# Optimization experiments

Measured on AMD Instinct MI355X. Metric: run time of the kernel, lower is better.

## Reference

```python
import jax, jax.numpy as jnp
import numpy as np

D = 1024
H = 16
FFN = 4096
B = 4
S = 1024
EPS = 1e-12
NEG = -1e9


def _layernorm(x, gamma, beta):
    mean = x.mean(-1, keepdims=True)
    var = ((x - mean) ** 2).mean(-1, keepdims=True)  # biased var, matches unbiased=False
    return gamma * (x - mean) * jax.lax.rsqrt(var + EPS) + beta


def setup_inputs() -> dict:
    key = jax.random.key(0)
    ks = jax.random.split(key, 16)
    s_in = 1.0 / np.sqrt(D)
    s_ff = 1.0 / np.sqrt(FFN)
    return {
        "x": jax.random.normal(ks[0], (B, S, D), dtype=jnp.float32),
        "mask": jax.random.randint(ks[1], (B, H, S), 0, 2) > 0,  # bernoulli(0.5) key mask
        "Wqkv": jax.random.uniform(ks[2], (3 * D, D), minval=-s_in, maxval=s_in),
        "bqkv": jax.random.uniform(ks[3], (3 * D,), minval=-s_in, maxval=s_in),
        "Wo": jax.random.uniform(ks[4], (D, D), minval=-s_in, maxval=s_in),
        "bo": jax.random.uniform(ks[5], (D,), minval=-s_in, maxval=s_in),
        "W1": jax.random.uniform(ks[6], (FFN, D), minval=-s_in, maxval=s_in),
        "b1": jax.random.uniform(ks[7], (FFN,), minval=-s_in, maxval=s_in),
        "W2": jax.random.uniform(ks[8], (D, FFN), minval=-s_ff, maxval=s_ff),
        "b2": jax.random.uniform(ks[9], (D,), minval=-s_ff, maxval=s_ff),
        "g1": jnp.ones((D,), jnp.float32),
        "be1": jnp.zeros((D,), jnp.float32),
        "g2": jnp.ones((D,), jnp.float32),
        "be2": jnp.zeros((D,), jnp.float32),
    }


def reference(x, mask, Wqkv, bqkv, Wo, bo, W1, b1, W2, b2, g1, be1, g2, be2):
    b, s, _ = x.shape
    hd = D // H
    scale = hd ** -0.5

    # --- ProbSparseSelfAttention (dropout in eval mode) ---
    qkv = x @ Wqkv.T + bqkv                                   # [b, s, 3D]
    q, k, v = jnp.split(qkv, 3, axis=-1)
    q = q.reshape(b, s, H, hd).transpose(0, 2, 1, 3)          # [b, h, s, d]
    k = k.reshape(b, s, H, hd).transpose(0, 2, 1, 3)
    v = v.reshape(b, s, H, hd).transpose(0, 2, 1, 3)
    scores = jnp.einsum('bhid,bhjd->bhij', q * scale, k)      # [b, h, s, s]
    scores = jnp.where(mask[:, :, None, :], scores, NEG)      # mask keys (broadcast over i)
    attn = jax.nn.softmax(scores, axis=-1)
    ctx = jnp.einsum('bhij,bhjd->bhid', attn, v)
    ctx = ctx.transpose(0, 2, 1, 3).reshape(b, s, D)
    attn_out = ctx @ Wo.T + bo

    # residual + LayerNorm 1
    h = _layernorm(attn_out + x, g1, be1)

    # --- FFN ---
    ff = jax.nn.relu(h @ W1.T + b1) @ W2.T + b2

    # residual + LayerNorm 2
    return _layernorm(ff + h, g2, be2)
```

## Files before the change

### kernel.cpp

```cpp
#include <hip/hip_runtime.h>

#define DDIM 1024
#define FFN_DIM 4096
#define SS 1024
#define MTOK 4096

typedef __bf16 bf16x8 __attribute__((ext_vector_type(8)));
typedef float f32x4 __attribute__((ext_vector_type(4)));
typedef unsigned short ushort4v __attribute__((ext_vector_type(4)));
typedef unsigned short ushort8v __attribute__((ext_vector_type(8)));

__device__ __forceinline__ unsigned short f2bf(float f) {
    union { float f; unsigned u; } x;
    x.f = f;
    unsigned r = x.u + 0x7FFFu + ((x.u >> 16) & 1u);
    return (unsigned short)(r >> 16);
}
__device__ __forceinline__ float bf2f(unsigned short u) {
    union { unsigned u; float f; } x;
    x.u = (unsigned)u << 16;
    return x.f;
}

__device__ __forceinline__ int swz(int off) {
    return off ^ ((((off >> 7) & 7) ^ ((off >> 10) & 1)) << 4);
}

__device__ __forceinline__ void gload_lds16(const void* g, void* l) {
    __builtin_amdgcn_global_load_lds(
        (__attribute__((address_space(1))) unsigned int*)(unsigned long long)(g),
        (__attribute__((address_space(3))) unsigned int*)(l), 16, 0, 0);
}

__global__ __launch_bounds__(256) void cvt_bf16(const float* __restrict__ in,
                                                unsigned short* __restrict__ out, int n4) {
    int i = blockIdx.x * 256 + threadIdx.x;
    if (i < n4) {
        float4 v = ((const float4*)in)[i];
        ushort4v u = {f2bf(v.x), f2bf(v.y), f2bf(v.z), f2bf(v.w)};
        ((ushort4v*)out)[i] = u;
    }
}

template <int EPI, int SPLITK>
__global__ __launch_bounds__(256) void gemm_bt(const unsigned short* __restrict__ A,
                                               const unsigned short* __restrict__ B,
                                               const float* __restrict__ bias,
                                               unsigned short* __restrict__ Cout,
                                               int M, int N, int K) {
    __shared__ unsigned short Asm[2][128 * 32];
    __shared__ unsigned short Bsm[2][128 * 32];
    const int tid = threadIdx.x;
    const int wid = tid >> 6, lane = tid & 63;
    const int m0 = blockIdx.y * 128, n0 = blockIdx.x * 128;
    const int lr = lane & 15, lk = (lane >> 4) * 8;
    const int wr = (wid >> 1) * 64, wc = (wid & 1) * 64;
    const int Kper = K / SPLITK;
    const int kbase = blockIdx.z * Kper;
    const int nkt = Kper / 32;

    f32x4 acc[4][4];
#pragma unroll
    for (int i = 0; i < 4; i++)
#pragma unroll
        for (int j = 0; j < 4; j++) acc[i][j] = (f32x4){0.f, 0.f, 0.f, 0.f};

    const unsigned short* Ag = A + (size_t)m0 * K;
    const unsigned short* Bg = B + (size_t)n0 * K;

    auto stage = [&](int buf, int k0) {
#pragma unroll
        for (int p = 0; p < 2; ++p) {
            int idx = p * 4096 + wid * 1024 + lane * 16;
            int row = idx >> 6, ce = (idx & 63) >> 1;
            gload_lds16(Ag + (size_t)row * K + k0 + ce, (char*)Asm[buf] + p * 4096 + wid * 1024);
            gload_lds16(Bg + (size_t)row * K + k0 + ce, (char*)Bsm[buf] + p * 4096 + wid * 1024);
        }
    };

    stage(0, kbase);
    for (int kt = 0; kt < nkt; ++kt) {
        const int cur = kt & 1;
        __syncthreads();
        if (kt + 1 < nkt) stage(cur ^ 1, kbase + (kt + 1) * 32);
        bf16x8 af[4], bfr[4];
#pragma unroll
        for (int m = 0; m < 4; m++) af[m] = *(const bf16x8*)&Asm[cur][(wr + m * 16 + lr) * 32 + lk];
#pragma unroll
        for (int n = 0; n < 4; n++) bfr[n] = *(const bf16x8*)&Bsm[cur][(wc + n * 16 + lr) * 32 + lk];
#pragma unroll
        for (int m = 0; m < 4; m++)
#pragma unroll
            for (int n = 0; n < 4; n++)
                acc[m][n] = __builtin_amdgcn_mfma_f32_16x16x32_bf16(af[m], bfr[n], acc[m][n], 0, 0, 0);
    }

    unsigned short* Op = Cout + (size_t)blockIdx.z * M * N;
    float bv[4];
    const bool hasb = (SPLITK == 1) || (blockIdx.z == 0);
#pragma unroll
    for (int n = 0; n < 4; n++) bv[n] = hasb ? bias[n0 + wc + n * 16 + lr] : 0.f;
    const int r0 = (lane >> 4) * 4;
#pragma unroll
    for (int m = 0; m < 4; m++) {
#pragma unroll
        for (int n = 0; n < 4; n++) {
            int col = n0 + wc + n * 16 + lr;
#pragma unroll
            for (int r = 0; r < 4; r++) {
                int row = m0 + wr + m * 16 + r0 + r;
                float v = acc[m][n][r] + bv[n];
                if (EPI == 2) v = fmaxf(v, 0.f);
                Op[(size_t)row * N + col] = f2bf(v);
            }
        }
    }
}

__global__ __launch_bounds__(256) void vtrans(const unsigned short* __restrict__ qkv,
                                              unsigned short* __restrict__ vt) {
    __shared__ unsigned short T[64 * 64];
    const int tid = threadIdx.x;
    const int bh = blockIdx.y, b = bh >> 4, h = bh & 15;
    const int s0 = blockIdx.x * 64;
    const unsigned short* src = qkv + (size_t)(b * SS + s0) * 3072 + 2048 + h * 64;
#pragma unroll
    for (int p = 0; p < 2; p++) {
        int idx = p * 4096 + tid * 16;
        int row = idx >> 7, ce = (idx & 127) >> 1;
        ushort8v v = *(const ushort8v*)(src + (size_t)row * 3072 + ce);
        *(ushort8v*)((char*)T + swz(idx)) = v;
    }
    __syncthreads();
    unsigned short* dst = vt + (size_t)bh * 64 * SS + s0;
#pragma unroll
    for (int p = 0; p < 2; p++) {
        int idx = p * 4096 + tid * 16;
        int d = idx >> 7, t0 = (idx & 127) >> 1;
        ushort8v o;
#pragma unroll
        for (int i = 0; i < 8; i++)
            o[i] = *(const unsigned short*)((char*)T + swz((t0 + i) * 128 + d * 2));
        *(ushort8v*)(dst + (size_t)d * SS + t0) = o;
    }
}

__global__ __launch_bounds__(256) void attn_fused(const unsigned short* __restrict__ qkv,
                                                  const unsigned short* __restrict__ vt,
                                                  const int* __restrict__ mask,
                                                  unsigned short* __restrict__ ctx) {
    __shared__ unsigned short Ksm[2][64 * 64];
    __shared__ unsigned short Vsm[2][64 * 64];
    __shared__ unsigned short Psm[4][16 * 64];
    __shared__ float maskadd[2][64];
    const int tid = threadIdx.x, wid = tid >> 6, lane = tid & 63;
    const int bh = blockIdx.y, b = bh >> 4, h = bh & 15;
    const int q0 = blockIdx.x * 64;
    const int lr = lane & 15, lk2 = (lane >> 4) * 16;
    const size_t base = (size_t)b * SS * 3072 + h * 64;

    bf16x8 qf[2];
    {
        const unsigned short* qp = qkv + base + (size_t)(q0 + wid * 16 + lr) * 3072;
        qf[0] = *(const bf16x8*)(qp + (lk2 >> 1));
        qf[1] = *(const bf16x8*)(qp + 32 + (lk2 >> 1));
    }
    float m_run[4] = {-3e38f, -3e38f, -3e38f, -3e38f};
    float l_run[4] = {0.f, 0.f, 0.f, 0.f};
    f32x4 oacc[4];
#pragma unroll
    for (int i = 0; i < 4; i++) oacc[i] = (f32x4){0.f, 0.f, 0.f, 0.f};

    const unsigned short* Kgb = qkv + base + 1024;
    const unsigned short* Vgb = vt + (size_t)bh * 64 * SS;

    auto stage = [&](int buf, int kt) {
#pragma unroll
        for (int p = 0; p < 2; p++) {
            int idx = p * 4096 + wid * 1024 + lane * 16;
            int s = swz(idx);
            int row = s >> 7, ce = (s & 127) >> 1;
            gload_lds16(Kgb + (size_t)(kt * 64 + row) * 3072 + ce,
                        (char*)Ksm[buf] + p * 4096 + wid * 1024);
            gload_lds16(Vgb + (size_t)row * SS + kt * 64 + ce,
                        (char*)Vsm[buf] + p * 4096 + wid * 1024);
        }
        if (tid < 64) maskadd[buf][tid] = mask[bh * SS + kt * 64 + tid] ? 0.f : -1e9f;
    };

    stage(0, 0);
    for (int kt = 0; kt < SS / 64; ++kt) {
        const int cur = kt & 1;
        __syncthreads();
        if (kt < SS / 64 - 1) stage(cur ^ 1, kt + 1);
        const char* Kb = (const char*)Ksm[cur];
        const char* Vb = (const char*)Vsm[cur];

        f32x4 sc[4];
#pragma unroll
        for (int nt = 0; nt < 4; nt++) {
            f32x4 a = (f32x4){0.f, 0.f, 0.f, 0.f};
            int rowb = (nt * 16 + lr) * 128;
            bf16x8 k0v = *(const bf16x8*)(Kb + swz(rowb + lk2));
            bf16x8 k1v = *(const bf16x8*)(Kb + swz(rowb + 64 + lk2));
            a = __builtin_amdgcn_mfma_f32_16x16x32_bf16(qf[0], k0v, a, 0, 0, 0);
            a = __builtin_amdgcn_mfma_f32_16x16x32_bf16(qf[1], k1v, a, 0, 0, 0);
            sc[nt] = a;
        }
        float mk[4];
#pragma unroll
        for (int nt = 0; nt < 4; nt++) mk[nt] = maskadd[cur][nt * 16 + lr];
#pragma unroll
        for (int r = 0; r < 4; r++) {
            float v = -3e38f;
#pragma unroll
            for (int nt = 0; nt < 4; nt++) {
                float s = sc[nt][r] * 0.125f + mk[nt];
                sc[nt][r] = s;
                v = fmaxf(v, s);
            }
            v = fmaxf(v, __shfl_xor(v, 1));
            v = fmaxf(v, __shfl_xor(v, 2));
            v = fmaxf(v, __shfl_xor(v, 4));
            v = fmaxf(v, __shfl_xor(v, 8));
            float mnew = fmaxf(m_run[r], v);
            float alpha = __expf(m_run[r] - mnew);
            m_run[r] = mnew;
            float ls = 0.f;
#pragma unroll
            for (int nt = 0; nt < 4; nt++) {
                float pexp = __expf(sc[nt][r] - mnew);
                sc[nt][r] = pexp;
                ls += pexp;
            }
            ls += __shfl_xor(ls, 1);
            ls += __shfl_xor(ls, 2);
            ls += __shfl_xor(ls, 4);
            ls += __shfl_xor(ls, 8);
            l_run[r] = l_run[r] * alpha + ls;
#pragma unroll
            for (int dt = 0; dt < 4; dt++) oacc[dt][r] *= alpha;
        }
        const int prow = (lane >> 4) * 4;
        char* Pb = (char*)Psm[wid];
#pragma unroll
        for (int nt = 0; nt < 4; nt++)
#pragma unroll
            for (int r = 0; r < 4; r++)
                *(unsigned short*)(Pb + swz((prow + r) * 128 + (nt * 16 + lr) * 2)) = f2bf(sc[nt][r]);
        bf16x8 pf0 = *(const bf16x8*)(Pb + swz(lr * 128 + lk2));
        bf16x8 pf1 = *(const bf16x8*)(Pb + swz(lr * 128 + 64 + lk2));
#pragma unroll
        for (int dt = 0; dt < 4; dt++) {
            int rowb = (dt * 16 + lr) * 128;
            bf16x8 v0 = *(const bf16x8*)(Vb + swz(rowb + lk2));
            bf16x8 v1 = *(const bf16x8*)(Vb + swz(rowb + 64 + lk2));
            oacc[dt] = __builtin_amdgcn_mfma_f32_16x16x32_bf16(pf0, v0, oacc[dt], 0, 0, 0);
            oacc[dt] = __builtin_amdgcn_mfma_f32_16x16x32_bf16(pf1, v1, oacc[dt], 0, 0, 0);
        }
    }
#pragma unroll
    for (int dt = 0; dt < 4; dt++) {
#pragma unroll
        for (int r = 0; r < 4; r++) {
            float v = oacc[dt][r] / l_run[r];
            int row = q0 + wid * 16 + (lane >> 4) * 4 + r;
            ctx[(size_t)(b * SS + row) * DDIM + h * 64 + dt * 16 + lr] = f2bf(v);
        }
    }
}

__global__ __launch_bounds__(256) void resid_ln1(const unsigned short* __restrict__ attno,
                                                 const float* __restrict__ x,
                                                 const float* __restrict__ gamma,
                                                 const float* __restrict__ beta,
                                                 unsigned short* __restrict__ hbf) {
    __shared__ float red[16];
    const int row = blockIdx.x, tid = threadIdx.x;
    const int wid = tid >> 6, lane = tid & 63;
    ushort4v av = ((const ushort4v*)(attno + (size_t)row * DDIM))[tid];
    float4 bv = ((const float4*)(x + (size_t)row * DDIM))[tid];
    float4 v;
    v.x = bf2f(av[0]) + bv.x; v.y = bf2f(av[1]) + bv.y;
    v.z = bf2f(av[2]) + bv.z; v.w = bf2f(av[3]) + bv.w;
    float s = v.x + v.y + v.z + v.w;
    float s2 = v.x * v.x + v.y * v.y + v.z * v.z + v.w * v.w;
#pragma unroll
    for (int off = 1; off < 64; off <<= 1) { s += __shfl_xor(s, off); s2 += __shfl_xor(s2, off); }
    if (lane == 0) { red[wid] = s; red[8 + wid] = s2; }
    __syncthreads();
    s = red[0] + red[1] + red[2] + red[3];
    s2 = red[8] + red[9] + red[10] + red[11];
    float mean = s * (1.f / 1024.f);
    float var = s2 * (1.f / 1024.f) - mean * mean;
    float rstd = rsqrtf(var + 1e-12f);
    float4 g = ((const float4*)gamma)[tid];
    float4 be = ((const float4*)beta)[tid];
    ushort4v u = {f2bf(g.x * (v.x - mean) * rstd + be.x),
                  f2bf(g.y * (v.y - mean) * rstd + be.y),
                  f2bf(g.z * (v.z - mean) * rstd + be.z),
                  f2bf(g.w * (v.w - mean) * rstd + be.w)};
    ((ushort4v*)(hbf + (size_t)row * DDIM))[tid] = u;
}

__global__ __launch_bounds__(256) void resid_ln2(const unsigned short* __restrict__ p0,
                                                 const unsigned short* __restrict__ p1,
                                                 const unsigned short* __restrict__ hbf,
                                                 const float* __restrict__ gamma,
                                                 const float* __restrict__ beta,
                                                 float* __restrict__ out) {
    __shared__ float red[16];
    const int row = blockIdx.x, tid = threadIdx.x;
    const int wid = tid >> 6, lane = tid & 63;
    ushort4v a0 = ((const ushort4v*)(p0 + (size_t)row * DDIM))[tid];
    ushort4v a1 = ((const ushort4v*)(p1 + (size_t)row * DDIM))[tid];
    ushort4v hv = ((const ushort4v*)(hbf + (size_t)row * DDIM))[tid];
    float4 v;
    v.x = bf2f(a0[0]) + bf2f(a1[0]) + bf2f(hv[0]);
    v.y = bf2f(a0[1]) + bf2f(a1[1]) + bf2f(hv[1]);
    v.z = bf2f(a0[2]) + bf2f(a1[2]) + bf2f(hv[2]);
    v.w = bf2f(a0[3]) + bf2f(a1[3]) + bf2f(hv[3]);
    float s = v.x + v.y + v.z + v.w;
    float s2 = v.x * v.x + v.y * v.y + v.z * v.z + v.w * v.w;
#pragma unroll
    for (int off = 1; off < 64; off <<= 1) { s += __shfl_xor(s, off); s2 += __shfl_xor(s2, off); }
    if (lane == 0) { red[wid] = s; red[8 + wid] = s2; }
    __syncthreads();
    s = red[0] + red[1] + red[2] + red[3];
    s2 = red[8] + red[9] + red[10] + red[11];
    float mean = s * (1.f / 1024.f);
    float var = s2 * (1.f / 1024.f) - mean * mean;
    float rstd = rsqrtf(var + 1e-12f);
    float4 g = ((const float4*)gamma)[tid];
    float4 be = ((const float4*)beta)[tid];
    float4 o;
    o.x = g.x * (v.x - mean) * rstd + be.x;
    o.y = g.y * (v.y - mean) * rstd + be.y;
    o.z = g.z * (v.z - mean) * rstd + be.z;
    o.w = g.w * (v.w - mean) * rstd + be.w;
    ((float4*)(out + (size_t)row * DDIM))[tid] = o;
}

extern "C" void kernel_launch(void* const* d_in, const int* in_sizes, int n_in,
                              void* d_out, int out_size, void* d_ws, size_t ws_size,
                              hipStream_t stream) {
    const float* x    = (const float*)d_in[0];
    const int*   mask = (const int*)d_in[1];
    const float* Wqkv = (const float*)d_in[2];
    const float* bqkv = (const float*)d_in[3];
    const float* Wo   = (const float*)d_in[4];
    const float* bo   = (const float*)d_in[5];
    const float* W1   = (const float*)d_in[6];
    const float* b1   = (const float*)d_in[7];
    const float* W2   = (const float*)d_in[8];
    const float* b2   = (const float*)d_in[9];
    const float* g1   = (const float*)d_in[10];
    const float* be1  = (const float*)d_in[11];
    const float* g2   = (const float*)d_in[12];
    const float* be2  = (const float*)d_in[13];
    float* out = (float*)d_out;

    char* ws = (char*)d_ws;
    unsigned short* xbf   = (unsigned short*)(ws + 0);
    unsigned short* vtb   = (unsigned short*)(ws + 0);
    unsigned short* qkvbf = (unsigned short*)(ws + (8ull << 20));
    unsigned short* ff1   = (unsigned short*)(ws + (8ull << 20));
    unsigned short* ctx   = (unsigned short*)(ws + (32ull << 20));
    unsigned short* w1b   = (unsigned short*)(ws + (40ull << 20));
    unsigned short* w2b   = (unsigned short*)(ws + (48ull << 20));
    unsigned short* wqkvb = (unsigned short*)(ws + (56ull << 20));
    unsigned short* wob   = (unsigned short*)(ws + (62ull << 20));
    unsigned short* attno = (unsigned short*)(ws + (64ull << 20));
    unsigned short* hbf   = (unsigned short*)(ws + (72ull << 20));
    unsigned short* pff   = (unsigned short*)(ws + (80ull << 20));

    cvt_bf16<<<4096, 256, 0, stream>>>(x, xbf, 1048576);
    cvt_bf16<<<3072, 256, 0, stream>>>(Wqkv, wqkvb, 786432);
    cvt_bf16<<<1024, 256, 0, stream>>>(Wo, wob, 262144);
    cvt_bf16<<<4096, 256, 0, stream>>>(W1, w1b, 1048576);
    cvt_bf16<<<4096, 256, 0, stream>>>(W2, w2b, 1048576);

    gemm_bt<1, 1><<<dim3(24, 32), 256, 0, stream>>>(xbf, wqkvb, bqkv, qkvbf, MTOK, 3072, 1024);
    vtrans<<<dim3(16, 64), 256, 0, stream>>>(qkvbf, vtb);
    attn_fused<<<dim3(16, 64), 256, 0, stream>>>(qkvbf, vtb, mask, ctx);
    gemm_bt<1, 1><<<dim3(8, 32), 256, 0, stream>>>(ctx, wob, bo, attno, MTOK, 1024, 1024);
    resid_ln1<<<4096, 256, 0, stream>>>(attno, x, g1, be1, hbf);
    gemm_bt<2, 1><<<dim3(32, 32), 256, 0, stream>>>(hbf, w1b, b1, ff1, MTOK, FFN_DIM, 1024);
    gemm_bt<1, 2><<<dim3(8, 32, 2), 256, 0, stream>>>(ff1, w2b, b2, pff, MTOK, 1024, FFN_DIM);
    resid_ln2<<<4096, 256, 0, stream>>>(pff, pff + (size_t)MTOK * DDIM, hbf, g2, be2, out);
}
```

Measured before the change: 382.1 us.

## Add 256x256 GEMM kernel, split-K 4 FFN2, XCD-aware attention with lazy rescale

Adds a 512-thread GEMM with 256x256 tiles and BK=64, swizzled LDS staging, interleaved prefetch and setprio around MFMA blocks. It is used for the QKV, FFN1 and FFN2 projections, with FFN2 split-K raised to 4 and partials written into reused workspace regions. Attention switches to a 1D grid remapped per XCD, uses exp2 with the scale folded in, and skips the online-softmax rescale unless the running max grows by more than 8. The larger tiles cut global traffic at the cost of more registers and LDS. Workspace aliasing for the split-K partials must not overlap any live buffer.

```diff
diff --git a/kernel.cpp b/kernel.cpp
--- a/kernel.cpp
+++ b/kernel.cpp
@@ -24,6 +24,9 @@
 
 __device__ __forceinline__ int swz(int off) {
     return off ^ ((((off >> 7) & 7) ^ ((off >> 10) & 1)) << 4);
+}
+__device__ __forceinline__ int gswz(int b) {
+    return b ^ (((b >> 7) & 7) << 4);
 }
 
 __device__ __forceinline__ void gload_lds16(const void* g, void* l) {
@@ -43,6 +46,114 @@
 }
 
 template <int EPI, int SPLITK>
+__global__ __launch_bounds__(512, 2) void gemm256(const unsigned short* __restrict__ A,
+                                                  const unsigned short* __restrict__ B,
+                                                  const float* __restrict__ bias,
+                                                  unsigned short* __restrict__ O0,
+                                                  unsigned short* __restrict__ O1,
+                                                  unsigned short* __restrict__ O2,
+                                                  unsigned short* __restrict__ O3,
+                                                  int M, int N, int K) {
+    __shared__ char smem[131072];
+    const int tid = threadIdx.x;
+    const int wid = tid >> 6, lane = tid & 63;
+    const int wm = wid >> 2, wn = wid & 3;
+    const int lr = lane & 15, lkb = (lane >> 4) * 16;
+    const int m0 = blockIdx.y * 256, n0 = blockIdx.x * 256;
+    const int z = blockIdx.z;
+    const int Kc = K / SPLITK, kb = z * Kc;
+    const int NT = Kc / 64;
+
+    f32x4 acc[8][4];
+#pragma unroll
+    for (int i = 0; i < 8; i++)
+#pragma unroll
+        for (int j = 0; j < 4; j++) acc[i][j] = (f32x4){0.f, 0.f, 0.f, 0.f};
+
+    auto stage_half = [&](int c, int t, int hs) {
+        const int op = hs >> 1, h = hs & 1;
+        const unsigned short* G = op ? B : A;
+        const int r0 = (op ? n0 : m0) + h * 128;
+        char* base = smem + c * 65536 + op * 32768 + h * 16384;
+        const int k0 = kb + t * 64;
+#pragma unroll
+        for (int q = 0; q < 2; q++) {
+            int d = q * 8192 + wid * 1024 + lane * 16;
+            int s = gswz(d);
+            int row = s >> 7, colb = s & 127;
+            gload_lds16(G + (size_t)(r0 + row) * K + k0 + (colb >> 1),
+                        base + q * 8192 + wid * 1024);
+        }
+    };
+
+    stage_half(0, 0, 0); stage_half(0, 0, 1); stage_half(0, 0, 2); stage_half(0, 0, 3);
+    asm volatile("s_waitcnt vmcnt(0)" ::: "memory");
+    __syncthreads();
+
+    for (int t = 0; t < NT; ++t) {
+        const int c = t & 1;
+        const char* Ab = smem + c * 65536;
+        const char* Bb = Ab + 32768;
+        const bool pre = (t + 1 < NT);
+        bf16x8 bfr[4][2];
+#pragma unroll
+        for (int p = 0; p < 4; ++p) {
+            bf16x8 afr[2][2];
+#pragma unroll
+            for (int mi = 0; mi < 2; mi++)
+#pragma unroll
+                for (int ks = 0; ks < 2; ks++) {
+                    int b = (wm * 128 + (p * 2 + mi) * 16 + lr) * 128 + ks * 64 + lkb;
+                    afr[mi][ks] = *(const bf16x8*)(Ab + gswz(b));
+                }
+            if (p == 0) {
+#pragma unroll
+                for (int nb = 0; nb < 4; nb++)
+#pragma unroll
+                    for (int ks = 0; ks < 2; ks++) {
+                        int b = (wn * 64 + nb * 16 + lr) * 128 + ks * 64 + lkb;
+                        bfr[nb][ks] = *(const bf16x8*)(Bb + gswz(b));
+                    }
+            }
+            if (pre) stage_half(c ^ 1, t + 1, p);
+            __builtin_amdgcn_s_barrier();
+            asm volatile("s_waitcnt lgkmcnt(0)" ::: "memory");
+            __builtin_amdgcn_sched_barrier(0);
+            __builtin_amdgcn_s_setprio(1);
+#pragma unroll
+            for (int mi = 0; mi < 2; mi++)
+#pragma unroll
+                for (int nb = 0; nb < 4; nb++)
+#pragma unroll
+                    for (int ks = 0; ks < 2; ks++)
+                        acc[p * 2 + mi][nb] = __builtin_amdgcn_mfma_f32_16x16x32_bf16(
+                            afr[mi][ks], bfr[nb][ks], acc[p * 2 + mi][nb], 0, 0, 0);
+            __builtin_amdgcn_s_setprio(0);
+            if (p == 3 && pre) asm volatile("s_waitcnt vmcnt(0)" ::: "memory");
+            __builtin_amdgcn_s_barrier();
+        }
+    }
+
+    unsigned short* Op = (SPLITK == 1) ? O0 : (z == 0 ? O0 : z == 1 ? O1 : z == 2 ? O2 : O3);
+    float bv[4];
+#pragma unroll
+    for (int nb = 0; nb < 4; nb++) bv[nb] = (z == 0) ? bias[n0 + wn * 64 + nb * 16 + lr] : 0.f;
+    const int rr = (lane >> 4) * 4;
+#pragma unroll
+    for (int mb = 0; mb < 8; mb++)
+#pragma unroll
+        for (int nb = 0; nb < 4; nb++) {
+            int col = n0 + wn * 64 + nb * 16 + lr;
+#pragma unroll
+            for (int r = 0; r < 4; r++) {
+                int row = m0 + wm * 128 + mb * 16 + rr + r;
+                float v = acc[mb][nb][r] + bv[nb];
+                if (EPI == 2) v = fmaxf(v, 0.f);
+                Op[(size_t)row * N + col] = f2bf(v);
+            }
+        }
+}
+
 __global__ __launch_bounds__(256) void gemm_bt(const unsigned short* __restrict__ A,
                                                const unsigned short* __restrict__ B,
                                                const float* __restrict__ bias,
@@ -55,9 +166,7 @@
     const int m0 = blockIdx.y * 128, n0 = blockIdx.x * 128;
     const int lr = lane & 15, lk = (lane >> 4) * 8;
     const int wr = (wid >> 1) * 64, wc = (wid & 1) * 64;
-    const int Kper = K / SPLITK;
-    const int kbase = blockIdx.z * Kper;
-    const int nkt = Kper / 32;
+    const int nkt = K / 32;
 
     f32x4 acc[4][4];
 #pragma unroll
@@ -78,11 +187,11 @@
         }
     };
 
-    stage(0, kbase);
+    stage(0, 0);
     for (int kt = 0; kt < nkt; ++kt) {
         const int cur = kt & 1;
         __syncthreads();
-        if (kt + 1 < nkt) stage(cur ^ 1, kbase + (kt + 1) * 32);
+        if (kt + 1 < nkt) stage(cur ^ 1, (kt + 1) * 32);
         bf16x8 af[4], bfr[4];
 #pragma unroll
         for (int m = 0; m < 4; m++) af[m] = *(const bf16x8*)&Asm[cur][(wr + m * 16 + lr) * 32 + lk];
@@ -95,26 +204,21 @@
                 acc[m][n] = __builtin_amdgcn_mfma_f32_16x16x32_bf16(af[m], bfr[n], acc[m][n], 0, 0, 0);
     }
 
-    unsigned short* Op = Cout + (size_t)blockIdx.z * M * N;
     float bv[4];
-    const bool hasb = (SPLITK == 1) || (blockIdx.z == 0);
-#pragma unroll
-    for (int n = 0; n < 4; n++) bv[n] = hasb ? bias[n0 + wc + n * 16 + lr] : 0.f;
+#pragma unroll
+    for (int n = 0; n < 4; n++) bv[n] = bias[n0 + wc + n * 16 + lr];
     const int r0 = (lane >> 4) * 4;
 #pragma unroll
-    for (int m = 0; m < 4; m++) {
+    for (int m = 0; m < 4; m++)
 #pragma unroll
         for (int n = 0; n < 4; n++) {
             int col = n0 + wc + n * 16 + lr;
 #pragma unroll
             for (int r = 0; r < 4; r++) {
                 int row = m0 + wr + m * 16 + r0 + r;
-                float v = acc[m][n][r] + bv[n];
-                if (EPI == 2) v = fmaxf(v, 0.f);
-                Op[(size_t)row * N + col] = f2bf(v);
+                Cout[(size_t)row * N + col] = f2bf(acc[m][n][r] + bv[n]);
             }
         }
-    }
 }
 
 __global__ __launch_bounds__(256) void vtrans(const unsigned short* __restrict__ qkv,
@@ -154,10 +258,13 @@
     __shared__ unsigned short Psm[4][16 * 64];
     __shared__ float maskadd[2][64];
     const int tid = threadIdx.x, wid = tid >> 6, lane = tid & 63;
-    const int bh = blockIdx.y, b = bh >> 4, h = bh & 15;
-    const int q0 = blockIdx.x * 64;
+    const int bid = blockIdx.x;
+    const int xcd = bid & 7, loc = bid >> 3;
+    const int bh = xcd * 8 + (loc >> 4), q0 = (loc & 15) * 64;
+    const int b = bh >> 4, h = bh & 15;
     const int lr = lane & 15, lk2 = (lane >> 4) * 16;
     const size_t base = (size_t)b * SS * 3072 + h * 64;
+    const float SC2 = 0.18033688011112042f;
 
     bf16x8 qf[2];
     {
@@ -185,7 +292,7 @@
             gload_lds16(Vgb + (size_t)row * SS + kt * 64 + ce,
                         (char*)Vsm[buf] + p * 4096 + wid * 1024);
         }
-        if (tid < 64) maskadd[buf][tid] = mask[bh * SS + kt * 64 + tid] ? 0.f : -1e9f;
+        if (tid < 64) maskadd[buf][tid] = mask[bh * SS + kt * 64 + tid] ? 0.f : -1.5e9f;
     };
 
     stage(0, 0);
@@ -210,12 +317,13 @@
         float mk[4];
 #pragma unroll
         for (int nt = 0; nt < 4; nt++) mk[nt] = maskadd[cur][nt * 16 + lr];
+        float pmax[4];
 #pragma unroll
         for (int r = 0; r < 4; r++) {
             float v = -3e38f;
 #pragma unroll
             for (int nt = 0; nt < 4; nt++) {
-                float s = sc[nt][r] * 0.125f + mk[nt];
+                float s = sc[nt][r] * SC2 + mk[nt];
                 sc[nt][r] = s;
                 v = fmaxf(v, s);
             }
@@ -223,13 +331,29 @@
             v = fmaxf(v, __shfl_xor(v, 2));
             v = fmaxf(v, __shfl_xor(v, 4));
             v = fmaxf(v, __shfl_xor(v, 8));
-            float mnew = fmaxf(m_run[r], v);
-            float alpha = __expf(m_run[r] - mnew);
-            m_run[r] = mnew;
+            pmax[r] = v;
+        }
+        bool okt = true;
+#pragma unroll
+        for (int r = 0; r < 4; r++) okt = okt && (pmax[r] <= m_run[r] + 8.f);
+        const bool skip = __all(okt);
+        if (!skip) {
+#pragma unroll
+            for (int r = 0; r < 4; r++) {
+                float mnew = fmaxf(m_run[r], pmax[r]);
+                float alpha = exp2f(m_run[r] - mnew);
+                m_run[r] = mnew;
+                l_run[r] *= alpha;
+#pragma unroll
+                for (int dt = 0; dt < 4; dt++) oacc[dt][r] *= alpha;
+            }
+        }
+#pragma unroll
+        for (int r = 0; r < 4; r++) {
             float ls = 0.f;
 #pragma unroll
             for (int nt = 0; nt < 4; nt++) {
-                float pexp = __expf(sc[nt][r] - mnew);
+                float pexp = exp2f(sc[nt][r] - m_run[r]);
                 sc[nt][r] = pexp;
                 ls += pexp;
             }
@@ -237,9 +361,7 @@
             ls += __shfl_xor(ls, 2);
             ls += __shfl_xor(ls, 4);
             ls += __shfl_xor(ls, 8);
-            l_run[r] = l_run[r] * alpha + ls;
-#pragma unroll
-            for (int dt = 0; dt < 4; dt++) oacc[dt][r] *= alpha;
+            l_run[r] += ls;
         }
         const int prow = (lane >> 4) * 4;
         char* Pb = (char*)Psm[wid];
@@ -260,14 +382,13 @@
         }
     }
 #pragma unroll
-    for (int dt = 0; dt < 4; dt++) {
+    for (int dt = 0; dt < 4; dt++)
 #pragma unroll
         for (int r = 0; r < 4; r++) {
             float v = oacc[dt][r] / l_run[r];
             int row = q0 + wid * 16 + (lane >> 4) * 4 + r;
             ctx[(size_t)(b * SS + row) * DDIM + h * 64 + dt * 16 + lr] = f2bf(v);
         }
-    }
 }
 
 __global__ __launch_bounds__(256) void resid_ln1(const unsigned short* __restrict__ attno,
@@ -305,6 +426,8 @@
 
 __global__ __launch_bounds__(256) void resid_ln2(const unsigned short* __restrict__ p0,
                                                  const unsigned short* __restrict__ p1,
+                                                 const unsigned short* __restrict__ p2,
+                                                 const unsigned short* __restrict__ p3,
                                                  const unsigned short* __restrict__ hbf,
                                                  const float* __restrict__ gamma,
                                                  const float* __restrict__ beta,
@@ -312,18 +435,21 @@
     __shared__ float red[16];
     const int row = blockIdx.x, tid = threadIdx.x;
     const int wid = tid >> 6, lane = tid & 63;
-    ushort4v a0 = ((const ushort4v*)(p0 + (size_t)row * DDIM))[tid];
-    ushort4v a1 = ((const ushort4v*)(p1 + (size_t)row * DDIM))[tid];
-    ushort4v hv = ((const ushort4v*)(hbf + (size_t)row * DDIM))[tid];
+    size_t off = (size_t)row * DDIM;
+    ushort4v a0 = ((const ushort4v*)(p0 + off))[tid];
+    ushort4v a1 = ((const ushort4v*)(p1 + off))[tid];
+    ushort4v a2 = ((const ushort4v*)(p2 + off))[tid];
+    ushort4v a3 = ((const ushort4v*)(p3 + off))[tid];
+    ushort4v hv = ((const ushort4v*)(hbf + off))[tid];
     float4 v;
-    v.x = bf2f(a0[0]) + bf2f(a1[0]) + bf2f(hv[0]);
-    v.y = bf2f(a0[1]) + bf2f(a1[1]) + bf2f(hv[1]);
-    v.z = bf2f(a0[2]) + bf2f(a1[2]) + bf2f(hv[2]);
-    v.w = bf2f(a0[3]) + bf2f(a1[3]) + bf2f(hv[3]);
+    v.x = bf2f(a0[0]) + bf2f(a1[0]) + bf2f(a2[0]) + bf2f(a3[0]) + bf2f(hv[0]);
+    v.y = bf2f(a0[1]) + bf2f(a1[1]) + bf2f(a2[1]) + bf2f(a3[1]) + bf2f(hv[1]);
+    v.z = bf2f(a0[2]) + bf2f(a1[2]) + bf2f(a2[2]) + bf2f(a3[2]) + bf2f(hv[2]);
+    v.w = bf2f(a0[3]) + bf2f(a1[3]) + bf2f(a2[3]) + bf2f(a3[3]) + bf2f(hv[3]);
     float s = v.x + v.y + v.z + v.w;
     float s2 = v.x * v.x + v.y * v.y + v.z * v.z + v.w * v.w;
 #pragma unroll
-    for (int off = 1; off < 64; off <<= 1) { s += __shfl_xor(s, off); s2 += __shfl_xor(s2, off); }
+    for (int off2 = 1; off2 < 64; off2 <<= 1) { s += __shfl_xor(s, off2); s2 += __shfl_xor(s2, off2); }
     if (lane == 0) { red[wid] = s; red[8 + wid] = s2; }
     __syncthreads();
     s = red[0] + red[1] + red[2] + red[3];
@@ -338,7 +464,7 @@
     o.y = g.y * (v.y - mean) * rstd + be.y;
     o.z = g.z * (v.z - mean) * rstd + be.z;
     o.w = g.w * (v.w - mean) * rstd + be.w;
-    ((float4*)(out + (size_t)row * DDIM))[tid] = o;
+    ((float4*)(out + off))[tid] = o;
 }
 
 extern "C" void kernel_launch(void* const* d_in, const int* in_sizes, int n_in,
@@ -363,16 +489,19 @@
     char* ws = (char*)d_ws;
     unsigned short* xbf   = (unsigned short*)(ws + 0);
     unsigned short* vtb   = (unsigned short*)(ws + 0);
+    unsigned short* p0    = (unsigned short*)(ws + 0);
     unsigned short* qkvbf = (unsigned short*)(ws + (8ull << 20));
     unsigned short* ff1   = (unsigned short*)(ws + (8ull << 20));
     unsigned short* ctx   = (unsigned short*)(ws + (32ull << 20));
     unsigned short* w1b   = (unsigned short*)(ws + (40ull << 20));
+    unsigned short* p1    = (unsigned short*)(ws + (40ull << 20));
     unsigned short* w2b   = (unsigned short*)(ws + (48ull << 20));
     unsigned short* wqkvb = (unsigned short*)(ws + (56ull << 20));
+    unsigned short* p2    = (unsigned short*)(ws + (56ull << 20));
     unsigned short* wob   = (unsigned short*)(ws + (62ull << 20));
     unsigned short* attno = (unsigned short*)(ws + (64ull << 20));
+    unsigned short* p3    = (unsigned short*)(ws + (64ull << 20));
     unsigned short* hbf   = (unsigned short*)(ws + (72ull << 20));
-    unsigned short* pff   = (unsigned short*)(ws + (80ull << 20));
 
     cvt_bf16<<<4096, 256, 0, stream>>>(x, xbf, 1048576);
     cvt_bf16<<<3072, 256, 0, stream>>>(Wqkv, wqkvb, 786432);
@@ -380,12 +509,15 @@
     cvt_bf16<<<4096, 256, 0, stream>>>(W1, w1b, 1048576);
     cvt_bf16<<<4096, 256, 0, stream>>>(W2, w2b, 1048576);
 
-    gemm_bt<1, 1><<<dim3(24, 32), 256, 0, stream>>>(xbf, wqkvb, bqkv, qkvbf, MTOK, 3072, 1024);
+    gemm256<1, 1><<<dim3(12, 16, 1), 512, 0, stream>>>(xbf, wqkvb, bqkv,
+        qkvbf, qkvbf, qkvbf, qkvbf, MTOK, 3072, 1024);
     vtrans<<<dim3(16, 64), 256, 0, stream>>>(qkvbf, vtb);
-    attn_fused<<<dim3(16, 64), 256, 0, stream>>>(qkvbf, vtb, mask, ctx);
-    gemm_bt<1, 1><<<dim3(8, 32), 256, 0, stream>>>(ctx, wob, bo, attno, MTOK, 1024, 1024);
+    attn_fused<<<1024, 256, 0, stream>>>(qkvbf, vtb, mask, ctx);
+    gemm_bt<<<dim3(8, 32), 256, 0, stream>>>(ctx, wob, bo, attno, MTOK, 1024, 1024);
     resid_ln1<<<4096, 256, 0, stream>>>(attno, x, g1, be1, hbf);
-    gemm_bt<2, 1><<<dim3(32, 32), 256, 0, stream>>>(hbf, w1b, b1, ff1, MTOK, FFN_DIM, 1024);
-    gemm_bt<1, 2><<<dim3(8, 32, 2), 256, 0, stream>>>(ff1, w2b, b2, pff, MTOK, 1024, FFN_DIM);
-    resid_ln2<<<4096, 256, 0, stream>>>(pff, pff + (size_t)MTOK * DDIM, hbf, g2, be2, out);
-}
+    gemm256<2, 1><<<dim3(16, 16, 1), 512, 0, stream>>>(hbf, w1b, b1,
+        ff1, ff1, ff1, ff1, MTOK, FFN_DIM, 1024);
+    gemm256<1, 4><<<dim3(4, 16, 4), 512, 0, stream>>>(ff1, w2b, b2,
+        p0, p1, p2, p3, MTOK, DDIM, FFN_DIM);
+    resid_ln2<<<4096, 256, 0, stream>>>(p0, p1, p2, p3, hbf, g2, be2, out);
+}
```

After: 372.2 us. 1.03x faster.
